# Optimization experiments

Measured on AMD Instinct MI355X. Metric: run time of the kernel, lower is better.

Reference implementation:

```python
import jax, jax.numpy as jnp
import numpy as np
import math

N, E, G = 10000, 100000, 500
HID, H = 128, 4
C = HID                      # out_channels per head (PyG TransformerConv)
NFREQ, NSPACE = 10, 3
EDIM = 2 * NFREQ * NSPACE    # 60 = dis_emb.dim
LAT, DIS = 6, 3
IN_DIM = HID + LAT + DIS     # 137
EPS = 1e-5


def _lin_init(k, fan_in, shape):
    b = 1.0 / math.sqrt(fan_in)
    return jax.random.uniform(k, shape, jnp.float32, -b, b)


def setup_inputs() -> dict:
    key = jax.random.key(0)
    ks = jax.random.split(key, 12)
    return dict(
        node_features=jax.random.normal(ks[0], (N, HID), jnp.float32),
        frac_coords=jax.random.uniform(ks[1], (N, DIS), jnp.float32),
        lattice_feats=jax.random.normal(ks[2], (G, LAT), jnp.float32),
        edge_index=jax.random.randint(ks[3], (2, E), 0, N),
        node2graph=jnp.sort(jax.random.randint(ks[4], (N,), 0, G)),
        frac_diff=jax.random.normal(ks[5], (E, DIS), jnp.float32) * 0.1,
        ln_gamma=jnp.ones((HID,), jnp.float32),
        ln_beta=jnp.zeros((HID,), jnp.float32),
        Wq=_lin_init(ks[6], IN_DIM, (IN_DIM, H * C)), bq=jnp.zeros((H * C,), jnp.float32),
        Wk=_lin_init(ks[7], IN_DIM, (IN_DIM, H * C)), bk=jnp.zeros((H * C,), jnp.float32),
        Wv=_lin_init(ks[8], IN_DIM, (IN_DIM, H * C)), bv=jnp.zeros((H * C,), jnp.float32),
        We=_lin_init(ks[9], EDIM, (EDIM, H * C)),
        Wskip=_lin_init(ks[10], IN_DIM, (IN_DIM, C)), bskip=jnp.zeros((C,), jnp.float32),
    )


def _sinusoids(frac_diff):
    # SinusoidsEmbedding: emb = x[...,None]*2*pi*arange(F); cat(sin, cos); detached
    freqs = 2.0 * jnp.pi * jnp.arange(NFREQ, dtype=jnp.float32)    # [F]
    emb = frac_diff[:, :, None] * freqs[None, None, :]             # [E,3,F]
    emb = emb.reshape(-1, NSPACE * NFREQ)                          # [E,30]
    return jnp.concatenate([jnp.sin(emb), jnp.cos(emb)], axis=-1)  # [E,60]


def _segment_softmax(scores, idx, num_segments):
    # softmax over variable-size neighborhoods grouped by target node idx
    m = jax.ops.segment_max(scores, idx, num_segments=num_segments)
    ex = jnp.exp(scores - m[idx])
    s = jax.ops.segment_sum(ex, idx, num_segments=num_segments)
    return ex / (s[idx] + 1e-16)


def reference(node_features, frac_coords, lattice_feats, edge_index, node2graph,
              frac_diff, ln_gamma, ln_beta, Wq, bq, Wk, bk, Wv, bv, We, Wskip, bskip):
    edge_emb = jax.lax.stop_gradient(_sinusoids(frac_diff))  # .detach() in original
    node_input = node_features
    # LayerNorm (biased variance, torch default)
    mu = node_features.mean(-1, keepdims=True)
    var = node_features.var(-1, keepdims=True)
    h = (node_features - mu) * jax.lax.rsqrt(var + EPS) * ln_gamma + ln_beta
    # gather per-graph lattice features to nodes, concat
    lat = lattice_feats.reshape(-1, LAT)[node2graph]                # [N,6]
    x = jnp.concatenate([h, lat, frac_coords], axis=1)              # [N,137]

    q = (x @ Wq + bq).reshape(N, H, C)
    k = (x @ Wk + bk).reshape(N, H, C)
    v = (x @ Wv + bv).reshape(N, H, C)
    e = (edge_emb @ We).reshape(E, H, C)                            # lin_edge (no bias)

    src, dst = edge_index[0], edge_index[1]  # message flows src -> dst (PyG default)
    k_e = k[src] + e                                                # [E,H,C]
    alpha = (q[dst] * k_e).sum(-1) / math.sqrt(C)                   # [E,H]
    alpha = _segment_softmax(alpha, dst, N)
    msg = (v[src] + e) * alpha[:, :, None]                          # [E,H,C]
    out = jax.ops.segment_sum(msg, dst, num_segments=N)             # [N,H,C]
    out = out.mean(axis=1)                                          # concat=False -> head mean
    out = out + (x @ Wskip + bskip)                                 # root skip connection
    return node_input + jax.nn.silu(out)
```

## Files before the change

kernel.cpp:

```cpp
#include <hip/hip_runtime.h>
#include <math.h>

#define N_NODES 10000
#define N_EDGES 100000
#define HIDDEN  128
#define NHEAD   4
#define CHAN    128
#define IN_DIM  137
#define KPAD    160
#define NCOLS   1904
#define NPAD    1920
#define LATD    6
#define DISD    3

#define PREP_BLOCKS 2500
#define WTOT   (NCOLS * KPAD + 4 * 128 * 64)
#define WBLOCKS ((WTOT + 255) / 256)

#define SCAT_BLOCKS ((N_EDGES + 255) / 256)
#define GEMM_BX 15
#define GEMM_BY ((N_NODES + 63) / 64)

typedef __attribute__((ext_vector_type(8))) short short8v;
typedef __attribute__((ext_vector_type(4))) float float4v;
typedef __attribute__((ext_vector_type(2))) float float2v;

__device__ inline unsigned short f2bf(float f) {
    unsigned u = __float_as_uint(f);
    unsigned r = 0x7fffu + ((u >> 16) & 1u);
    return (unsigned short)((u + r) >> 16);
}
__device__ inline float bf2f(unsigned short u) {
    return __uint_as_float(((unsigned)u) << 16);
}

__global__ __launch_bounds__(256) void prep_weights_kernel(
    const float* __restrict__ nf, const float* __restrict__ frac,
    const float* __restrict__ lat, const int* __restrict__ n2g,
    const float* __restrict__ gamma, const float* __restrict__ beta,
    const float* __restrict__ Wq, const float* __restrict__ bq,
    const float* __restrict__ Wk, const float* __restrict__ bk,
    const float* __restrict__ Wv, const float* __restrict__ bv,
    const float* __restrict__ Wsk, const float* __restrict__ bsk,
    const float* __restrict__ We,
    unsigned short* __restrict__ xb, int* __restrict__ hist,
    unsigned short* __restrict__ wallT, float* __restrict__ bias_all,
    unsigned short* __restrict__ webt)
{
    if (blockIdx.x < PREP_BLOCKS) {
        int wave = threadIdx.x >> 6;
        int lane = threadIdx.x & 63;
        int n = blockIdx.x * 4 + wave;
        if (n >= N_NODES) return;

        float v0 = nf[n * HIDDEN + lane];
        float v1 = nf[n * HIDDEN + 64 + lane];
        float s  = v0 + v1;
        float sq = v0 * v0 + v1 * v1;
        #pragma unroll
        for (int m = 1; m < 64; m <<= 1) {
            s  += __shfl_xor(s, m);
            sq += __shfl_xor(sq, m);
        }
        float mean = s * (1.0f / 128.0f);
        float var  = sq * (1.0f / 128.0f) - mean * mean;
        float inv  = rsqrtf(var + 1e-5f);

        xb[n * KPAD + lane]      = f2bf((v0 - mean) * inv * gamma[lane]      + beta[lane]);
        xb[n * KPAD + 64 + lane] = f2bf((v1 - mean) * inv * gamma[64 + lane] + beta[64 + lane]);
        if (lane < LATD) xb[n * KPAD + HIDDEN + lane]        = f2bf(lat[n2g[n] * LATD + lane]);
        if (lane < DISD) xb[n * KPAD + HIDDEN + LATD + lane] = f2bf(frac[n * DISD + lane]);
        if (lane >= 41)  xb[n * KPAD + 96 + lane] = 0;
        if (lane == 0)   hist[n] = 0;
    } else {
        int idx = (blockIdx.x - PREP_BLOCKS) * 256 + threadIdx.x;
        if (idx >= WTOT) return;
        if (idx < NCOLS * KPAD) {
            int n = idx / KPAD, k = idx % KPAD;
            if (n < 1664) {
                float val = 0.0f;
                if (k < IN_DIM) {
                    if (n < 512)        val = Wq[(size_t)k * 512 + n];
                    else if (n < 1024)  val = Wk[(size_t)k * 512 + (n - 512)];
                    else if (n < 1536)  val = Wv[(size_t)k * 512 + (n - 1024)];
                    else                val = Wsk[(size_t)k * 128 + (n - 1536)];
                }
                wallT[idx] = f2bf(val);
                if (k == 0) {
                    float b;
                    if (n < 512)        b = bq[n];
                    else if (n < 1024)  b = bk[n - 512];
                    else if (n < 1536)  b = bv[n - 1024];
                    else                b = bsk[n - 1536];
                    bias_all[n] = b;
                }
            } else {
                int hj = n - 1664;
                int h = hj / 60, j = hj % 60;
                float s = 0.0f;
                if (k < IN_DIM) {
                    #pragma unroll 4
                    for (int c = 0; c < 128; ++c)
                        s += Wq[(size_t)k * 512 + h * 128 + c] * We[(size_t)j * 512 + h * 128 + c];
                }
                wallT[idx] = f2bf(s);
                if (k == KPAD - 1) {
                    float b = 0.0f;
                    #pragma unroll 4
                    for (int c = 0; c < 128; ++c)
                        b += bq[h * 128 + c] * We[(size_t)j * 512 + h * 128 + c];
                    bias_all[n] = b;
                }
            }
        } else {
            int g = idx - NCOLS * KPAD;
            int h = g >> 13, c = (g >> 6) & 127, j = g & 63;
            float v = (j < 60) ? We[(size_t)j * 512 + h * 128 + c] : 0.0f;
            webt[g] = f2bf(v);
        }
    }
}

__global__ __launch_bounds__(256) void hist_kernel(
    const int* __restrict__ eidx, int* __restrict__ hist)
{
    int e = blockIdx.x * 256 + threadIdx.x;
    if (e < N_EDGES) atomicAdd(&hist[eidx[N_EDGES + e]], 1);
}

__global__ __launch_bounds__(1024) void scan_kernel(
    const int* __restrict__ hist, int* __restrict__ offsets, int* __restrict__ cursor)
{
    __shared__ int part[1024];
    const int t = threadIdx.x;
    const int base = t * 10;
    int loc[10];
    int s = 0;
    #pragma unroll
    for (int i = 0; i < 10; ++i) {
        int v = (base + i < N_NODES) ? hist[base + i] : 0;
        loc[i] = s; s += v;
    }
    part[t] = s;
    __syncthreads();
    for (int off = 1; off < 1024; off <<= 1) {
        int v = (t >= off) ? part[t - off] : 0;
        __syncthreads();
        part[t] += v;
        __syncthreads();
    }
    int pre = (t > 0) ? part[t - 1] : 0;
    #pragma unroll
    for (int i = 0; i < 10; ++i)
        if (base + i < N_NODES) {
            offsets[base + i] = pre + loc[i];
            cursor[base + i]  = pre + loc[i];
        }
    if (t == 1023) offsets[N_NODES] = part[1023];
}

__global__ __launch_bounds__(256) void gemm_scatter_kernel(
    const unsigned short* __restrict__ xb, const unsigned short* __restrict__ wallT,
    const float* __restrict__ bias_all,
    const int* __restrict__ eidx, const float* __restrict__ fdiff,
    int* __restrict__ cursor, int* __restrict__ sorted_src,
    float* __restrict__ sorted_fd,
    float* __restrict__ sq, unsigned short* __restrict__ qbuf,
    unsigned char* __restrict__ kvb)
{
    __shared__ __align__(16) unsigned short Alds[64 * 168];

    if (blockIdx.x < SCAT_BLOCKS) {
        int e = blockIdx.x * 256 + threadIdx.x;
        if (e >= N_EDGES) return;
        int src = eidx[e];
        int dst = eidx[N_EDGES + e];
        int pos = atomicAdd(&cursor[dst], 1);
        sorted_src[pos] = src;
        sorted_fd[pos * 3 + 0] = fdiff[e * 3 + 0];
        sorted_fd[pos * 3 + 1] = fdiff[e * 3 + 1];
        sorted_fd[pos * 3 + 2] = fdiff[e * 3 + 2];
        return;
    }

    const int bx   = blockIdx.x - SCAT_BLOCKS;
    const int row0 = (bx / GEMM_BX) * 64;
    const int col0 = (bx % GEMM_BX) * 128;
    const int tid  = threadIdx.x;

    for (int i = tid; i < 64 * 20; i += 256) {
        int r = i / 20, c8 = (i % 20) * 8;
        uint4 v = make_uint4(0u, 0u, 0u, 0u);
        if (row0 + r < N_NODES)
            v = *reinterpret_cast<const uint4*>(&xb[(size_t)(row0 + r) * KPAD + c8]);
        *reinterpret_cast<uint4*>(&Alds[r * 168 + c8]) = v;
    }
    __syncthreads();

    const int l   = tid & 63;
    const int wid = tid >> 6;
    const int wr  = (wid >> 1) * 32;
    const int wc  = (wid & 1) * 64;
    const int lr  = l & 15;
    const int lk  = (l >> 4) * 8;

    float4v acc[2][4];
    #pragma unroll
    for (int tr = 0; tr < 2; ++tr)
        #pragma unroll
        for (int tc = 0; tc < 4; ++tc)
            acc[tr][tc] = (float4v){0.0f, 0.0f, 0.0f, 0.0f};

    #pragma unroll
    for (int ks = 0; ks < 5; ++ks) {
        short8v a[2], b[4];
        #pragma unroll
        for (int t = 0; t < 2; ++t)
            a[t] = *reinterpret_cast<const short8v*>(&Alds[(wr + t * 16 + lr) * 168 + ks * 32 + lk]);
        #pragma unroll
        for (int t = 0; t < 4; ++t)
            b[t] = *reinterpret_cast<const short8v*>(
                &wallT[(size_t)(col0 + wc + t * 16 + lr) * KPAD + ks * 32 + lk]);
        #pragma unroll
        for (int tr = 0; tr < 2; ++tr)
            #pragma unroll
            for (int tc = 0; tc < 4; ++tc)
                acc[tr][tc] = __builtin_amdgcn_mfma_f32_16x16x32_bf16(a[tr], b[tc], acc[tr][tc], 0, 0, 0);
    }

    #pragma unroll
    for (int tr = 0; tr < 2; ++tr) {
        #pragma unroll
        for (int tc = 0; tc < 4; ++tc) {
            const int col  = col0 + wc + tc * 16 + lr;
            const float bias = bias_all[col];
            #pragma unroll
            for (int j = 0; j < 4; ++j) {
                const int row = row0 + wr + tr * 16 + (l >> 4) * 4 + j;
                if (row < N_NODES) {
                    float val = acc[tr][tc][j] + bias;
                    if (col < 512) {
                        qbuf[(size_t)row * 512 + col] = f2bf(val);
                    } else if (col < 1024) {
                        const int h = (col - 512) >> 7, ck = (col - 512) & 127;
                        int p = __builtin_amdgcn_cvt_pk_fp8_f32(val, val, 0, false);
                        kvb[((size_t)row * 4 + h) * 384 + ck] = (unsigned char)(p & 0xFF);
                    } else if (col < 1536) {
                        const int h = (col - 1024) >> 7, cv = (col - 1024) & 127;
                        *reinterpret_cast<unsigned short*>(
                            kvb + ((size_t)row * 4 + h) * 384 + 128 + 2 * cv) = f2bf(val);
                    } else if (col < 1664) {
                        sq[(size_t)row * 384 + (col - 1536)] = val;
                    } else if (col < NCOLS) {
                        sq[(size_t)row * 384 + 128 + (col - 1664)] = val;
                    }
                }
            }
        }
    }
}

__global__ __launch_bounds__(256) void gather_kernel(
    const float* __restrict__ sq, const unsigned short* __restrict__ qbuf,
    const unsigned char* __restrict__ kvb,
    const int* __restrict__ offsets, const int* __restrict__ sorted_src,
    const float* __restrict__ sorted_fd,
    float* __restrict__ avbuf, unsigned short* __restrict__ aggbuf,
    float* __restrict__ sumwbuf)
{
    const int n    = blockIdx.x;
    const int h    = threadIdx.x >> 6;
    const int l    = threadIdx.x & 63;
    const int hl   = l & 31;
    const int half = l >> 5;
    const float TWO_PI = 6.283185307179586f;
    const float scale  = 0.08838834764831845f;

    const ushort4 qv = *reinterpret_cast<const ushort4*>(
        &qbuf[(size_t)n * 512 + h * 128 + 4 * hl]);
    const float q4x = bf2f(qv.x), q4y = bf2f(qv.y);
    const float q4z = bf2f(qv.z), q4w = bf2f(qv.w);
    const float qe_a = sq[(size_t)n * 384 + 128 + h * 60 + hl];
    const bool  v2ok = (hl < 28);
    const float qe_b = v2ok ? sq[(size_t)n * 384 + 128 + h * 60 + hl + 32] : 0.0f;

    const int   jj1  = (hl < 30) ? hl : hl - 30;
    const int   sd1  = jj1 / 10;
    const float fc1  = TWO_PI * (float)(jj1 % 10);
    const bool  sin1 = (hl < 30);
    const int   jj2  = hl + 2;
    const int   sd2  = v2ok ? (jj2 / 10) : 0;
    const float fc2  = v2ok ? TWO_PI * (float)(jj2 % 10) : 0.0f;

    float ax = 0.f, ay = 0.f, az = 0.f, aw = 0.f;
    float agg1 = 0.f, agg2 = 0.f, sumw = 0.f;
    const int e0 = offsets[n], e1 = offsets[n + 1];

    for (int base = e0; base < e1; base += 4) {
        const int eA = base + half;
        const int eB = base + half + 2;
        const bool okA = (eA < e1), okB = (eB < e1);
        const int iA = okA ? eA : e0;
        const int iB = okB ? eB : e0;
        const int srcA = sorted_src[iA];
        const int srcB = sorted_src[iB];
        const float fdA1 = sorted_fd[iA * 3 + sd1];
        const float fdA2 = sorted_fd[iA * 3 + sd2];
        const float fdB1 = sorted_fd[iB * 3 + sd1];
        const float fdB2 = sorted_fd[iB * 3 + sd2];
        const unsigned char* pA = kvb + ((size_t)srcA * 4 + h) * 384;
        const unsigned char* pB = kvb + ((size_t)srcB * 4 + h) * 384;
        const unsigned kAu = *reinterpret_cast<const unsigned*>(pA + 4 * hl);
        const ushort4  vA  = *reinterpret_cast<const ushort4*>(pA + 128 + 8 * hl);
        const unsigned kBu = *reinterpret_cast<const unsigned*>(pB + 4 * hl);
        const ushort4  vB  = *reinterpret_cast<const ushort4*>(pB + 128 + 8 * hl);

        const float eA1 = sin1 ? __sinf(fdA1 * fc1) : __cosf(fdA1 * fc1);
        const float eA2 = __cosf(fdA2 * fc2);
        const float eB1 = sin1 ? __sinf(fdB1 * fc1) : __cosf(fdB1 * fc1);
        const float eB2 = __cosf(fdB2 * fc2);

        const float2v kA01 = __builtin_amdgcn_cvt_pk_f32_fp8(kAu, false);
        const float2v kA23 = __builtin_amdgcn_cvt_pk_f32_fp8(kAu, true);
        const float2v kB01 = __builtin_amdgcn_cvt_pk_f32_fp8(kBu, false);
        const float2v kB23 = __builtin_amdgcn_cvt_pk_f32_fp8(kBu, true);

        float pAs = q4x * kA01[0] + q4y * kA01[1]
                  + q4z * kA23[0] + q4w * kA23[1]
                  + eA1 * qe_a + eA2 * qe_b;
        float pBs = q4x * kB01[0] + q4y * kB01[1]
                  + q4z * kB23[0] + q4w * kB23[1]
                  + eB1 * qe_a + eB2 * qe_b;
        #pragma unroll
        for (int m = 1; m <= 16; m <<= 1) {
            pAs += __shfl_xor(pAs, m);
            pBs += __shfl_xor(pBs, m);
        }
        const float wA = okA ? __expf(pAs * scale) : 0.0f;
        const float wB = okB ? __expf(pBs * scale) : 0.0f;
        sumw += wA + wB;
        ax += wA * bf2f(vA.x) + wB * bf2f(vB.x);
        ay += wA * bf2f(vA.y) + wB * bf2f(vB.y);
        az += wA * bf2f(vA.z) + wB * bf2f(vB.z);
        aw += wA * bf2f(vA.w) + wB * bf2f(vB.w);
        agg1 += wA * eA1 + wB * eB1;
        if (v2ok) agg2 += wA * eA2 + wB * eB2;
    }

    sumw += __shfl_xor(sumw, 32);
    ax += __shfl_xor(ax, 32);  ay += __shfl_xor(ay, 32);
    az += __shfl_xor(az, 32);  aw += __shfl_xor(aw, 32);
    agg1 += __shfl_xor(agg1, 32);
    agg2 += __shfl_xor(agg2, 32);

    if (half == 0) {
        float4 r;
        r.x = ax; r.y = ay; r.z = az; r.w = aw;
        *reinterpret_cast<float4*>(&avbuf[(size_t)n * 512 + h * 128 + 4 * hl]) = r;
        aggbuf[n * 256 + h * 64 + hl]      = f2bf(agg1);
        aggbuf[n * 256 + h * 64 + 32 + hl] = f2bf(agg2);
        if (hl == 0) sumwbuf[n * 4 + h] = sumw;
    }
}

__global__ __launch_bounds__(256) void corr_kernel(
    const unsigned short* __restrict__ webt, const unsigned short* __restrict__ aggbuf,
    float* __restrict__ avbuf)
{
    __shared__ __align__(16) unsigned short Alds[32 * 264];
    const int node0 = blockIdx.x * 32;
    const int tid = threadIdx.x;

    for (int i = tid; i < 32 * 32; i += 256) {
        int r = i >> 5, c8 = (i & 31) * 8;
        uint4 v = make_uint4(0u, 0u, 0u, 0u);
        if (node0 + r < N_NODES)
            v = *reinterpret_cast<const uint4*>(&aggbuf[(size_t)(node0 + r) * 256 + c8]);
        *reinterpret_cast<uint4*>(&Alds[r * 264 + c8]) = v;
    }
    __syncthreads();

    const int l  = tid & 63;
    const int h  = tid >> 6;
    const int lr = l & 15;
    const int lk = (l >> 4) * 8;

    float4v acc[2][8];
    #pragma unroll
    for (int m = 0; m < 2; ++m)
        #pragma unroll
        for (int nn = 0; nn < 8; ++nn)
            acc[m][nn] = (float4v){0.0f, 0.0f, 0.0f, 0.0f};

    #pragma unroll
    for (int ks = 0; ks < 2; ++ks) {
        short8v a[2], b[8];
        #pragma unroll
        for (int m = 0; m < 2; ++m)
            a[m] = *reinterpret_cast<const short8v*>(
                &Alds[(m * 16 + lr) * 264 + h * 64 + ks * 32 + lk]);
        #pragma unroll
        for (int nn = 0; nn < 8; ++nn)
            b[nn] = *reinterpret_cast<const short8v*>(
                &webt[(size_t)(h * 128 + nn * 16 + lr) * 64 + ks * 32 + lk]);
        #pragma unroll
        for (int m = 0; m < 2; ++m)
            #pragma unroll
            for (int nn = 0; nn < 8; ++nn)
                acc[m][nn] = __builtin_amdgcn_mfma_f32_16x16x32_bf16(a[m], b[nn], acc[m][nn], 0, 0, 0);
    }

    #pragma unroll
    for (int m = 0; m < 2; ++m) {
        #pragma unroll
        for (int nn = 0; nn < 8; ++nn) {
            const int col = h * 128 + nn * 16 + lr;
            #pragma unroll
            for (int j = 0; j < 4; ++j) {
                const int rowi = node0 + m * 16 + (l >> 4) * 4 + j;
                if (rowi < N_NODES) {
                    float* p = &avbuf[(size_t)rowi * 512 + col];
                    *p += acc[m][nn][j];
                }
            }
        }
    }
}

__global__ __launch_bounds__(256) void finalize_kernel(
    const float* __restrict__ avbuf, const float* __restrict__ sumwbuf,
    const float* __restrict__ sq, const float* __restrict__ nf,
    float* __restrict__ out)
{
    int idx = blockIdx.x * 256 + threadIdx.x;
    if (idx >= N_NODES * CHAN) return;
    int n = idx >> 7, c = idx & 127;
    float z = 0.0f;
    #pragma unroll
    for (int h = 0; h < NHEAD; ++h)
        z += avbuf[(size_t)n * 512 + h * 128 + c] / (sumwbuf[n * 4 + h] + 1e-16f);
    z = 0.25f * z + sq[(size_t)n * 384 + c];
    float si = z / (1.0f + __expf(-z));
    out[idx] = nf[idx] + si;
}

extern "C" void kernel_launch(void* const* d_in, const int* in_sizes, int n_in,
                              void* d_out, int out_size, void* d_ws, size_t ws_size,
                              hipStream_t stream)
{
    const float* nf    = (const float*)d_in[0];
    const float* frac  = (const float*)d_in[1];
    const float* lat   = (const float*)d_in[2];
    const int*   eidx  = (const int*)  d_in[3];
    const int*   n2g   = (const int*)  d_in[4];
    const float* fdiff = (const float*)d_in[5];
    const float* gamma = (const float*)d_in[6];
    const float* beta  = (const float*)d_in[7];
    const float* Wq    = (const float*)d_in[8];
    const float* bq    = (const float*)d_in[9];
    const float* Wk    = (const float*)d_in[10];
    const float* bk    = (const float*)d_in[11];
    const float* Wv    = (const float*)d_in[12];
    const float* bv    = (const float*)d_in[13];
    const float* We    = (const float*)d_in[14];
    const float* Wsk   = (const float*)d_in[15];
    const float* bsk   = (const float*)d_in[16];
    float* out = (float*)d_out;

    float* sq        = (float*)d_ws;
    float* avbuf     = sq + (size_t)N_NODES * 384;
    float* sumwbuf   = avbuf + (size_t)N_NODES * 512;
    float* bias_all  = sumwbuf + (size_t)N_NODES * 4;
    float* sorted_fd = bias_all + NPAD;
    unsigned short* xb     = (unsigned short*)(sorted_fd + (size_t)N_EDGES * 3);
    unsigned short* wallT  = xb + (size_t)N_NODES * KPAD;
    unsigned short* webt   = wallT + (size_t)NPAD * KPAD;
    unsigned short* aggbuf = webt + 4 * 128 * 64;
    unsigned short* qbuf   = aggbuf + (size_t)N_NODES * 256;
    unsigned char*  kvb    = (unsigned char*)(qbuf + (size_t)N_NODES * 512);
    int* hist       = (int*)(kvb + (size_t)N_NODES * 4 * 384);
    int* offsets    = hist + N_NODES;
    int* cursor     = offsets + N_NODES + 1;
    int* sorted_src = cursor + N_NODES;

    prep_weights_kernel<<<PREP_BLOCKS + WBLOCKS, 256, 0, stream>>>(
        nf, frac, lat, n2g, gamma, beta,
        Wq, bq, Wk, bk, Wv, bv, Wsk, bsk, We,
        xb, hist, wallT, bias_all, webt);

    hist_kernel<<<(N_EDGES + 255) / 256, 256, 0, stream>>>(eidx, hist);
    scan_kernel<<<1, 1024, 0, stream>>>(hist, offsets, cursor);

    gemm_scatter_kernel<<<SCAT_BLOCKS + GEMM_BX * GEMM_BY, 256, 0, stream>>>(
        xb, wallT, bias_all, eidx, fdiff, cursor, sorted_src, sorted_fd,
        sq, qbuf, kvb);

    gather_kernel<<<N_NODES, 256, 0, stream>>>(
        sq, qbuf, kvb, offsets, sorted_src, sorted_fd, avbuf, aggbuf, sumwbuf);

    corr_kernel<<<(N_NODES + 31) / 32, 256, 0, stream>>>(webt, aggbuf, avbuf);

    finalize_kernel<<<(N_NODES * CHAN + 255) / 256, 256, 0, stream>>>(
        avbuf, sumwbuf, sq, nf, out);
}
```

Before: 148.3 us.

## Store V in fp8 alongside K and transpose weights through LDS tiles

The value projection is now stored as fp8 instead of bf16, which shrinks the per-node-head K/V record from 384 to 256 bytes and halves the V bytes gathered per edge in the attention kernel. Separately, the weight-transpose part of the prep kernel now stages 64-column tiles in shared memory so the reads from the weight matrices are coalesced and the bf16 rows are written as 16-byte vectors. The Wq·We fold and the We transpose are given their own block ranges. The fp8 V adds quantisation error to the aggregated messages, which may affect accuracy tolerance.

Measured after the change: 141.1 us. 4.8% less time.

```diff
diff --git a/kernel.cpp b/kernel.cpp
--- a/kernel.cpp
+++ b/kernel.cpp
@@ -14,8 +14,9 @@
 #define DISD    3
 
 #define PREP_BLOCKS 2500
-#define WTOT   (NCOLS * KPAD + 4 * 128 * 64)
-#define WBLOCKS ((WTOT + 255) / 256)
+#define TRANS_TILES 26
+#define WQE_BLOCKS  150
+#define WEBT_BLOCKS 128
 
 #define SCAT_BLOCKS ((N_EDGES + 255) / 256)
 #define GEMM_BX 15
@@ -47,9 +48,12 @@
     unsigned short* __restrict__ wallT, float* __restrict__ bias_all,
     unsigned short* __restrict__ webt)
 {
+    __shared__ __align__(16) unsigned short Tlds[64 * 168];
+    const int tid = threadIdx.x;
+
     if (blockIdx.x < PREP_BLOCKS) {
-        int wave = threadIdx.x >> 6;
-        int lane = threadIdx.x & 63;
+        int wave = tid >> 6;
+        int lane = tid & 63;
         int n = blockIdx.x * 4 + wave;
         if (n >= N_NODES) return;
 
@@ -72,52 +76,60 @@
         if (lane < DISD) xb[n * KPAD + HIDDEN + LATD + lane] = f2bf(frac[n * DISD + lane]);
         if (lane >= 41)  xb[n * KPAD + 96 + lane] = 0;
         if (lane == 0)   hist[n] = 0;
+    } else if (blockIdx.x < PREP_BLOCKS + TRANS_TILES) {
+        const int n0 = (blockIdx.x - PREP_BLOCKS) * 64;
+        for (int i = tid; i < 160 * 64; i += 256) {
+            const int k = i >> 6, n = i & 63;
+            const int col = n0 + n;
+            float val = 0.0f;
+            if (k < IN_DIM) {
+                if (col < 512)        val = Wq[(size_t)k * 512 + col];
+                else if (col < 1024)  val = Wk[(size_t)k * 512 + (col - 512)];
+                else if (col < 1536)  val = Wv[(size_t)k * 512 + (col - 1024)];
+                else                  val = Wsk[(size_t)k * 128 + (col - 1536)];
+            }
+            Tlds[n * 168 + k] = f2bf(val);
+        }
+        __syncthreads();
+        for (int i = tid; i < 64 * 20; i += 256) {
+            const int n = i / 20, c8 = (i % 20) * 8;
+            *reinterpret_cast<uint4*>(&wallT[(size_t)(n0 + n) * KPAD + c8]) =
+                *reinterpret_cast<const uint4*>(&Tlds[n * 168 + c8]);
+        }
+        if (tid < 64) {
+            const int col = n0 + tid;
+            float b;
+            if (col < 512)        b = bq[col];
+            else if (col < 1024)  b = bk[col - 512];
+            else if (col < 1536)  b = bv[col - 1024];
+            else                  b = bsk[col - 1536];
+            bias_all[col] = b;
+        }
+    } else if (blockIdx.x < PREP_BLOCKS + TRANS_TILES + WQE_BLOCKS) {
+        int idx = (blockIdx.x - PREP_BLOCKS - TRANS_TILES) * 256 + tid;
+        if (idx >= 240 * KPAD) return;
+        int hj = idx / KPAD, k = idx % KPAD;
+        int h = hj / 60, j = hj % 60;
+        float s = 0.0f;
+        if (k < IN_DIM) {
+            #pragma unroll 4
+            for (int c = 0; c < 128; ++c)
+                s += Wq[(size_t)k * 512 + h * 128 + c] * We[(size_t)j * 512 + h * 128 + c];
+        }
+        wallT[(size_t)(1664 + hj) * KPAD + k] = f2bf(s);
+        if (k == KPAD - 1) {
+            float b = 0.0f;
+            #pragma unroll 4
+            for (int c = 0; c < 128; ++c)
+                b += bq[h * 128 + c] * We[(size_t)j * 512 + h * 128 + c];
+            bias_all[1664 + hj] = b;
+        }
     } else {
-        int idx = (blockIdx.x - PREP_BLOCKS) * 256 + threadIdx.x;
-        if (idx >= WTOT) return;
-        if (idx < NCOLS * KPAD) {
-            int n = idx / KPAD, k = idx % KPAD;
-            if (n < 1664) {
-                float val = 0.0f;
-                if (k < IN_DIM) {
-                    if (n < 512)        val = Wq[(size_t)k * 512 + n];
-                    else if (n < 1024)  val = Wk[(size_t)k * 512 + (n - 512)];
-                    else if (n < 1536)  val = Wv[(size_t)k * 512 + (n - 1024)];
-                    else                val = Wsk[(size_t)k * 128 + (n - 1536)];
-                }
-                wallT[idx] = f2bf(val);
-                if (k == 0) {
-                    float b;
-                    if (n < 512)        b = bq[n];
-                    else if (n < 1024)  b = bk[n - 512];
-                    else if (n < 1536)  b = bv[n - 1024];
-                    else                b = bsk[n - 1536];
-                    bias_all[n] = b;
-                }
-            } else {
-                int hj = n - 1664;
-                int h = hj / 60, j = hj % 60;
-                float s = 0.0f;
-                if (k < IN_DIM) {
-                    #pragma unroll 4
-                    for (int c = 0; c < 128; ++c)
-                        s += Wq[(size_t)k * 512 + h * 128 + c] * We[(size_t)j * 512 + h * 128 + c];
-                }
-                wallT[idx] = f2bf(s);
-                if (k == KPAD - 1) {
-                    float b = 0.0f;
-                    #pragma unroll 4
-                    for (int c = 0; c < 128; ++c)
-                        b += bq[h * 128 + c] * We[(size_t)j * 512 + h * 128 + c];
-                    bias_all[n] = b;
-                }
-            }
-        } else {
-            int g = idx - NCOLS * KPAD;
-            int h = g >> 13, c = (g >> 6) & 127, j = g & 63;
-            float v = (j < 60) ? We[(size_t)j * 512 + h * 128 + c] : 0.0f;
-            webt[g] = f2bf(v);
-        }
+        int g = (blockIdx.x - PREP_BLOCKS - TRANS_TILES - WQE_BLOCKS) * 256 + tid;
+        if (g >= 4 * 128 * 64) return;
+        int h = g >> 13, c = (g >> 6) & 127, j = g & 63;
+        float v = (j < 60) ? We[(size_t)j * 512 + h * 128 + c] : 0.0f;
+        webt[g] = f2bf(v);
     }
 }
 
@@ -244,11 +256,11 @@
                     } else if (col < 1024) {
                         const int h = (col - 512) >> 7, ck = (col - 512) & 127;
                         int p = __builtin_amdgcn_cvt_pk_fp8_f32(val, val, 0, false);
-                        kvb[((size_t)row * 4 + h) * 384 + ck] = (unsigned char)(p & 0xFF);
+                        kvb[((size_t)row * 4 + h) * 256 + ck] = (unsigned char)(p & 0xFF);
                     } else if (col < 1536) {
                         const int h = (col - 1024) >> 7, cv = (col - 1024) & 127;
-                        *reinterpret_cast<unsigned short*>(
-                            kvb + ((size_t)row * 4 + h) * 384 + 128 + 2 * cv) = f2bf(val);
+                        int p = __builtin_amdgcn_cvt_pk_fp8_f32(val, val, 0, false);
+                        kvb[((size_t)row * 4 + h) * 256 + 128 + cv] = (unsigned char)(p & 0xFF);
                     } else if (col < 1664) {
                         sq[(size_t)row * 384 + (col - 1536)] = val;
                     } else if (col < NCOLS) {
@@ -308,12 +320,12 @@
         const float fdA2 = sorted_fd[iA * 3 + sd2];
         const float fdB1 = sorted_fd[iB * 3 + sd1];
         const float fdB2 = sorted_fd[iB * 3 + sd2];
-        const unsigned char* pA = kvb + ((size_t)srcA * 4 + h) * 384;
-        const unsigned char* pB = kvb + ((size_t)srcB * 4 + h) * 384;
+        const unsigned char* pA = kvb + ((size_t)srcA * 4 + h) * 256;
+        const unsigned char* pB = kvb + ((size_t)srcB * 4 + h) * 256;
         const unsigned kAu = *reinterpret_cast<const unsigned*>(pA + 4 * hl);
-        const ushort4  vA  = *reinterpret_cast<const ushort4*>(pA + 128 + 8 * hl);
+        const unsigned vAu = *reinterpret_cast<const unsigned*>(pA + 128 + 4 * hl);
         const unsigned kBu = *reinterpret_cast<const unsigned*>(pB + 4 * hl);
-        const ushort4  vB  = *reinterpret_cast<const ushort4*>(pB + 128 + 8 * hl);
+        const unsigned vBu = *reinterpret_cast<const unsigned*>(pB + 128 + 4 * hl);
 
         const float eA1 = sin1 ? __sinf(fdA1 * fc1) : __cosf(fdA1 * fc1);
         const float eA2 = __cosf(fdA2 * fc2);
@@ -339,10 +351,15 @@
         const float wA = okA ? __expf(pAs * scale) : 0.0f;
         const float wB = okB ? __expf(pBs * scale) : 0.0f;
         sumw += wA + wB;
-        ax += wA * bf2f(vA.x) + wB * bf2f(vB.x);
-        ay += wA * bf2f(vA.y) + wB * bf2f(vB.y);
-        az += wA * bf2f(vA.z) + wB * bf2f(vB.z);
-        aw += wA * bf2f(vA.w) + wB * bf2f(vB.w);
+
+        const float2v vA01 = __builtin_amdgcn_cvt_pk_f32_fp8(vAu, false);
+        const float2v vA23 = __builtin_amdgcn_cvt_pk_f32_fp8(vAu, true);
+        const float2v vB01 = __builtin_amdgcn_cvt_pk_f32_fp8(vBu, false);
+        const float2v vB23 = __builtin_amdgcn_cvt_pk_f32_fp8(vBu, true);
+        ax += wA * vA01[0] + wB * vB01[0];
+        ay += wA * vA01[1] + wB * vB01[1];
+        az += wA * vA23[0] + wB * vB23[0];
+        aw += wA * vA23[1] + wB * vB23[1];
         agg1 += wA * eA1 + wB * eB1;
         if (v2ok) agg2 += wA * eA2 + wB * eB2;
     }
@@ -478,12 +495,13 @@
     unsigned short* aggbuf = webt + 4 * 128 * 64;
     unsigned short* qbuf   = aggbuf + (size_t)N_NODES * 256;
     unsigned char*  kvb    = (unsigned char*)(qbuf + (size_t)N_NODES * 512);
-    int* hist       = (int*)(kvb + (size_t)N_NODES * 4 * 384);
+    int* hist       = (int*)(kvb + (size_t)N_NODES * 4 * 256);
     int* offsets    = hist + N_NODES;
     int* cursor     = offsets + N_NODES + 1;
     int* sorted_src = cursor + N_NODES;
 
-    prep_weights_kernel<<<PREP_BLOCKS + WBLOCKS, 256, 0, stream>>>(
+    prep_weights_kernel<<<PREP_BLOCKS + TRANS_TILES + WQE_BLOCKS + WEBT_BLOCKS,
+                          256, 0, stream>>>(
         nf, frac, lat, n2g, gamma, beta,
         Wq, bq, Wk, bk, Wv, bv, Wsk, bsk, We,
         xb, hist, wallT, bias_all, webt);
```
